# Kernel optimization log

Hardware: AMD Instinct MI355X
Metric: run time of the kernel (lower is better)

## Reference

```python
import jax, jax.numpy as jnp
import numpy as np
from math import comb

# Module hyperparameters (init_kwargs)
B_, C_, H_, W_, M_, N_ = 256, 3, 256, 256, 31, 31


def _bernstein(num_samples: int, deg: int) -> np.ndarray:
    """Bernstein basis evaluated at pixel-center points t_i=(i+0.5)/num_samples.
    Returns (num_samples, deg+1): C(deg,k) * t^k * (1-t)^(deg-k)."""
    t = (np.arange(num_samples, dtype=np.float64) + 0.5) / num_samples
    k = np.arange(deg + 1)
    coeff = np.array([comb(deg, i) for i in range(deg + 1)], dtype=np.float64)
    basis = coeff * (t[:, None] ** k) * ((1.0 - t[:, None]) ** (deg - k))
    return basis.astype(np.float32)


def _bez_basis() -> np.ndarray:
    # Full separable basis, matching bez_filter: (H, W, M+1, N+1)
    bu = _bernstein(H_, M_)  # (H, M+1)
    bv = _bernstein(W_, N_)  # (W, N+1)
    return bu[:, None, :, None] * bv[None, :, None, :]


_BASIS = jnp.asarray(_bez_basis())  # (H, W, M+1, N+1) constant, not trainable


def setup_inputs() -> dict:
    key = jax.random.key(0)
    K_mat = jax.random.normal(key, (B_, C_, M_ + 1, N_ + 1), dtype=jnp.float32) * 0.05
    x = jnp.zeros((1,), dtype=jnp.int32)  # `inputs` is ignored by the layer
    return {"x": x, "K_mat": K_mat}


def reference(x, K_mat):
    # out[b,c,i,j] = sum_{p,q} K_mat[b,c,p,q] * basis[i,j,p,q]
    # Single batched GEMM replacing b*c tiny conv2d launches.
    out = jnp.einsum('bcpq,hwpq->bchw', K_mat, _BASIS)
    return out[None]  # (1, b, c, h, w) per compute_output_shape
```

## Files before the change

### kernel.cpp

```cpp
#include <hip/hip_runtime.h>


#define DEG 31

__global__ __launch_bounds__(256) void bez_basis_kernel(float* __restrict__ B) {
    int g = blockIdx.x * 256 + threadIdx.x;
    int i = g >> 5;
    int k = g & 31;
    double t = ((double)i + 0.5) / 256.0;
    double coeff = 1.0;
    for (int kk = 1; kk <= k; ++kk)
        coeff = coeff * (double)(DEG - kk + 1) / (double)kk;
    double tk = 1.0;
    for (int e = 0; e < k; ++e) tk *= t;
    double omt = 1.0 - t;
    double tq = 1.0;
    for (int e = 0; e < DEG - k; ++e) tq *= omt;
    B[g] = (float)(coeff * tk * tq);
}

__global__ __launch_bounds__(256) void bez_main_kernel(
        const float* __restrict__ K,
        const float* __restrict__ B,
        float* __restrict__ out) {
    const int bc  = blockIdx.x;
    const int tid = threadIdx.x;

    float breg[32];
    const float4* brow = (const float4*)(B + tid * 32);
    #pragma unroll
    for (int q4 = 0; q4 < 8; ++q4) {
        float4 v = brow[q4];
        breg[q4 * 4 + 0] = v.x;
        breg[q4 * 4 + 1] = v.y;
        breg[q4 * 4 + 2] = v.z;
        breg[q4 * 4 + 3] = v.w;
    }

    const float* Kbc = K + (size_t)bc * 1024;
    float treg[32];
    #pragma unroll
    for (int p = 0; p < 32; ++p) {
        float acc = 0.0f;
        #pragma unroll
        for (int q = 0; q < 32; ++q)
            acc += Kbc[p * 32 + q] * breg[q];
        treg[p] = acc;
    }

    float* outbc = out + (size_t)bc * 65536;
    #pragma unroll 4
    for (int i = 0; i < 256; ++i) {
        const float* bu = B + i * 32;
        float acc = 0.0f;
        #pragma unroll
        for (int p = 0; p < 32; ++p)
            acc += bu[p] * treg[p];
        outbc[i * 256 + tid] = acc;
    }
}

extern "C" void kernel_launch(void* const* d_in, const int* in_sizes, int n_in,
                              void* d_out, int out_size, void* d_ws, size_t ws_size,
                              hipStream_t stream) {
    const float* K = (const float*)d_in[1];
    float* B   = (float*)d_ws;
    float* out = (float*)d_out;

    bez_basis_kernel<<<dim3(32), dim3(256), 0, stream>>>(B);
    bez_main_kernel<<<dim3(768), dim3(256), 0, stream>>>(K, B, out);
}
```

Baseline: 252.6 us.

## Use split-bf16 MFMA for the second basis contraction stage

```diff
diff --git a/kernel.cpp b/kernel.cpp
--- a/kernel.cpp
+++ b/kernel.cpp
@@ -3,7 +3,22 @@
 
 #define DEG 31
 
-__global__ __launch_bounds__(256) void bez_basis_kernel(float* __restrict__ B) {
+typedef short bf16x8 __attribute__((ext_vector_type(8)));
+typedef float f32x4  __attribute__((ext_vector_type(4)));
+
+__device__ __forceinline__ unsigned short f2bf_rne(float x) {
+    unsigned int u = __float_as_uint(x);
+    unsigned int r = (u + 0x7FFFu + ((u >> 16) & 1u)) >> 16;
+    return (unsigned short)r;
+}
+__device__ __forceinline__ float bf2f(unsigned short h) {
+    return __uint_as_float(((unsigned int)h) << 16);
+}
+
+__global__ __launch_bounds__(256) void bez_basis_kernel(
+        float* __restrict__ Bt,
+        unsigned short* __restrict__ Hi,
+        unsigned short* __restrict__ Lo) {
     int g = blockIdx.x * 256 + threadIdx.x;
     int i = g >> 5;
     int k = g & 31;
@@ -16,18 +31,29 @@
     double omt = 1.0 - t;
     double tq = 1.0;
     for (int e = 0; e < DEG - k; ++e) tq *= omt;
-    B[g] = (float)(coeff * tk * tq);
+    float v = (float)(coeff * tk * tq);
+    Bt[g] = v;
+    unsigned short h = f2bf_rne(v);
+    Hi[g] = h;
+    Lo[g] = f2bf_rne(v - bf2f(h));
 }
 
 __global__ __launch_bounds__(256) void bez_main_kernel(
         const float* __restrict__ K,
-        const float* __restrict__ B,
+        const float* __restrict__ Bt,
+        const unsigned short* __restrict__ Hi,
+        const unsigned short* __restrict__ Lo,
         float* __restrict__ out) {
-    const int bc  = blockIdx.x;
-    const int tid = threadIdx.x;
+    __shared__ __align__(16) unsigned short sBhi[256 * 32];
+    __shared__ __align__(16) unsigned short sBlo[256 * 32];
+
+    const int bc   = blockIdx.x;
+    const int tid  = threadIdx.x;
+    const int lane = tid & 63;
+    const int w    = tid >> 6;
 
     float breg[32];
-    const float4* brow = (const float4*)(B + tid * 32);
+    const float4* brow = (const float4*)(Bt + tid * 32);
     #pragma unroll
     for (int q4 = 0; q4 < 8; ++q4) {
         float4 v = brow[q4];
@@ -36,7 +62,6 @@
         breg[q4 * 4 + 2] = v.z;
         breg[q4 * 4 + 3] = v.w;
     }
-
     const float* Kbc = K + (size_t)bc * 1024;
     float treg[32];
     #pragma unroll
@@ -47,16 +72,52 @@
             acc += Kbc[p * 32 + q] * breg[q];
         treg[p] = acc;
     }
+    #pragma unroll
+    for (int c = 0; c < 4; ++c) {
+        bf16x8 vh, vl;
+        #pragma unroll
+        for (int jj = 0; jj < 8; ++jj) {
+            float x = treg[c * 8 + jj];
+            unsigned short h = f2bf_rne(x);
+            vh[jj] = (short)h;
+            vl[jj] = (short)f2bf_rne(x - bf2f(h));
+        }
+        int boff = (tid * 4 + (c ^ (tid & 3))) * 8;
+        *(bf16x8*)&sBhi[boff] = vh;
+        *(bf16x8*)&sBlo[boff] = vl;
+    }
+    __syncthreads();
+
+    const int m = lane & 15;
+    const int q = lane >> 4;
+
+    bf16x8 Ah[4], Al[4];
+    #pragma unroll
+    for (int a = 0; a < 4; ++a) {
+        int row = (w * 4 + a) * 16 + m;
+        Ah[a] = *(const bf16x8*)(Hi + row * 32 + q * 8);
+        Al[a] = *(const bf16x8*)(Lo + row * 32 + q * 8);
+    }
 
     float* outbc = out + (size_t)bc * 65536;
-    #pragma unroll 4
-    for (int i = 0; i < 256; ++i) {
-        const float* bu = B + i * 32;
-        float acc = 0.0f;
+    for (int tj = 0; tj < 16; ++tj) {
+        int n = tj * 16 + m;
+        int boff = (n * 4 + (q ^ (n & 3))) * 8;
+        bf16x8 Bh = *(const bf16x8*)&sBhi[boff];
+        bf16x8 Bl = *(const bf16x8*)&sBlo[boff];
         #pragma unroll
-        for (int p = 0; p < 32; ++p)
-            acc += bu[p] * treg[p];
-        outbc[i * 256 + tid] = acc;
+        for (int a = 0; a < 4; ++a) {
+            f32x4 acc = {0.0f, 0.0f, 0.0f, 0.0f};
+            acc = __builtin_amdgcn_mfma_f32_16x16x32_bf16(Al[a], Bh, acc, 0, 0, 0);
+            acc = __builtin_amdgcn_mfma_f32_16x16x32_bf16(Ah[a], Bl, acc, 0, 0, 0);
+            acc = __builtin_amdgcn_mfma_f32_16x16x32_bf16(Ah[a], Bh, acc, 0, 0, 0);
+            int row0 = (w * 4 + a) * 16 + q * 4;
+            float* o = outbc + row0 * 256 + tj * 16 + m;
+            o[0]   = acc[0];
+            o[256] = acc[1];
+            o[512] = acc[2];
+            o[768] = acc[3];
+        }
     }
 }
 
@@ -64,9 +125,12 @@
                               void* d_out, int out_size, void* d_ws, size_t ws_size,
                               hipStream_t stream) {
     const float* K = (const float*)d_in[1];
-    float* B   = (float*)d_ws;
+    char* ws = (char*)d_ws;
+    float*          Bt = (float*)ws;
+    unsigned short* Hi = (unsigned short*)(ws + 32768);
+    unsigned short* Lo = (unsigned short*)(ws + 49152);
     float* out = (float*)d_out;
 
-    bez_basis_kernel<<<dim3(32), dim3(256), 0, stream>>>(B);
-    bez_main_kernel<<<dim3(768), dim3(256), 0, stream>>>(K, B, out);
+    bez_basis_kernel<<<dim3(32), dim3(256), 0, stream>>>(Bt, Hi, Lo);
+    bez_main_kernel<<<dim3(768), dim3(256), 0, stream>>>(K, Bt, Hi, Lo, out);
 }
```

Result: faster. 219.1 us (-13.3%).
